# Kernel optimization log

Measured on AMD Instinct MI355X. Metric: run time of the kernel, lower is better.

## Reference

```python
import jax, jax.numpy as jnp
import numpy as np

HEADS = 4

def _axial_attn(xs, wqkv, wproj, bproj, heads=HEADS):
    # xs: [B', C, L]; wqkv: [3C, C]; wproj: [C, C]; bproj: [C]
    Bp, C, L = xs.shape
    hd = C // heads
    scale = hd ** -0.5
    qkv = jnp.einsum('oc,bcl->bol', wqkv, xs)  # [B', 3C, L]
    q, k, v = jnp.split(qkv, 3, axis=1)
    q = q.reshape(Bp, heads, hd, L)
    k = k.reshape(Bp, heads, hd, L)
    v = v.reshape(Bp, heads, hd, L)
    attn = jax.nn.softmax(jnp.einsum('bhdi,bhdj->bhij', q, k) * scale, axis=-1)
    out = jnp.einsum('bhij,bhdj->bhdi', attn, v).reshape(Bp, C, L)
    return jnp.einsum('oc,bcl->bol', wproj, out) + bproj[None, :, None]

def setup_inputs() -> dict:
    key = jax.random.key(0)
    ks = jax.random.split(key, 7)
    B, C, H, W = 8, 128, 128, 128
    return {
        'x': jax.random.normal(ks[0], (B, C, H, W), dtype=jnp.float32),
        'wqkv_h': jax.random.normal(ks[1], (3 * C, C), dtype=jnp.float32) * 0.05,
        'wproj_h': jax.random.normal(ks[2], (C, C), dtype=jnp.float32) * 0.05,
        'bproj_h': jax.random.normal(ks[3], (C,), dtype=jnp.float32) * 0.05,
        'wqkv_w': jax.random.normal(ks[4], (3 * C, C), dtype=jnp.float32) * 0.05,
        'wproj_w': jax.random.normal(ks[5], (C, C), dtype=jnp.float32) * 0.05,
        'bproj_w': jax.random.normal(ks[6], (C,), dtype=jnp.float32) * 0.05,
    }

def reference(x, wqkv_h, wproj_h, bproj_h, wqkv_w, wproj_w, bproj_w):
    B, C, H, W = x.shape
    # height pass: rows become batch, attend along W
    xh = x.transpose(0, 2, 1, 3).reshape(B * H, C, W)
    xh = _axial_attn(xh, wqkv_h, wproj_h, bproj_h)
    xh = xh.reshape(B, H, C, W).transpose(0, 2, 1, 3)
    # width pass: cols become batch, attend along H
    xw = x.transpose(0, 3, 1, 2).reshape(B * W, C, H)
    xw = _axial_attn(xw, wqkv_w, wproj_w, bproj_w)
    xw = xw.reshape(B, W, C, H).transpose(0, 2, 3, 1)
    return (xh + xw) / 2
```

## Files before the change

### kernel.cpp

```cpp
#include <hip/hip_runtime.h>
#include <hip/hip_bf16.h>
#include <stdint.h>

typedef __attribute__((ext_vector_type(8))) short short8v;
typedef __attribute__((ext_vector_type(4))) float f32x4;
typedef unsigned short u16;
typedef unsigned int u32;

__device__ __align__(16) u16 g_xTw[8u * 128u * 128u * 128u];
__device__ __align__(16) u16 g_W1 [8u * 128u * 128u * 128u];
__device__ __align__(16) u16 g_W2 [8u * 128u * 128u * 128u];
__device__ __align__(16) u16 g_wqkvP[2u * 49152u];
__device__ __align__(16) u16 g_wpP [2u * 16384u];

#define XST_OFF 0
#define QT_OFF  32768
#define KT_OFF  43008
#define VH_OFF  53248
#define OT_OFF  61952
#define SMEM_BYTES 72192

__device__ __forceinline__ u16 f2bf(float f) {
    u32 b = __float_as_uint(f);
    b += 0x7FFFu + ((b >> 16) & 1u);
    return (u16)(b >> 16);
}
__device__ __forceinline__ u32 pk2(float a, float b) {
    __hip_bfloat162 h = __float22bfloat162_rn(make_float2(a, b));
    union { __hip_bfloat162 h; u32 u; } cv; cv.h = h; return cv.u;
}
__device__ __forceinline__ float bf2f(u16 u) {
    return __uint_as_float(((u32)u) << 16);
}

__global__ __launch_bounds__(512)
void prep_weights(const float* __restrict__ wqkv_h, const float* __restrict__ wproj_h,
                  const float* __restrict__ wqkv_w, const float* __restrict__ wproj_w)
{
    const float QSC = 0.17677669529663687f;
    int id = blockIdx.x * 512 + threadIdx.x;
    if (id < 12288) {
        int p = id / 6144, i2 = id % 6144;
        int h = i2 / 1536, i3 = i2 % 1536;
        int t = i3 / 256,  i4 = i3 % 256;
        int kk = i4 / 64,  lane = i4 % 64;
        int cc = lane & 15, qq = lane >> 4;
        int r96 = t * 16 + cc;
        int g = r96 >> 5, rl = r96 & 31;
        const float* src = (p == 0 ? wqkv_h : wqkv_w) + (g * 128 + h * 32 + rl) * 128 + kk * 32 + qq * 8;
        float4 a = *(const float4*)src;
        float4 c = *(const float4*)(src + 4);
        float s = (g == 0) ? QSC : 1.0f;
        *(uint4*)(g_wqkvP + (size_t)id * 8) =
            make_uint4(pk2(a.x * s, a.y * s), pk2(a.z * s, a.w * s),
                       pk2(c.x * s, c.y * s), pk2(c.z * s, c.w * s));
    } else {
        int id2 = id - 12288;
        int p = id2 / 2048, i2 = id2 % 2048;
        int h = i2 / 512,  i3 = i2 % 512;
        int t = i3 / 64,   lane = i3 % 64;
        int cc = lane & 15, qq = lane >> 4;
        int o = t * 16 + cc;
        const float* src = (p == 0 ? wproj_h : wproj_w) + o * 128 + h * 32 + qq * 8;
        float4 a = *(const float4*)src;
        float4 c = *(const float4*)(src + 4);
        *(uint4*)(g_wpP + (size_t)id2 * 8) =
            make_uint4(pk2(a.x, a.y), pk2(a.z, a.w), pk2(c.x, c.y), pk2(c.z, c.w));
    }
}

__global__ __launch_bounds__(256)
void transpose_x(const float* __restrict__ x)
{
    __shared__ char tsm[32768];
    const int b = blockIdx.x >> 6;
    const int hp = blockIdx.x & 63;
    const int tid = threadIdx.x;
    for (int hh = 0; hh < 2; ++hh) {
        const int h = hp * 2 + hh;
        #pragma unroll
        for (int it = 0; it < 16; ++it) {
            int task = it * 256 + tid;
            int w = task & 127, c4 = task >> 7;
            const float* p = x + (size_t)b * 2097152 + (c4 * 4) * 16384 + h * 128 + w;
            u32 u0 = pk2(p[0], p[16384]);
            u32 u1 = pk2(p[2 * 16384], p[3 * 16384]);
            int off = w * 256 + ((((c4 >> 1) << 4) ^ ((w & 7) << 4)) | ((c4 & 1) << 3));
            *(uint2*)(tsm + off) = make_uint2(u0, u1);
        }
        __syncthreads();
        #pragma unroll
        for (int it = 0; it < 8; ++it) {
            int i = it * 256 + tid;
            int w = i >> 4, c8 = i & 15;
            uint4 v = *(const uint4*)(tsm + w * 256 + ((c8 << 4) ^ ((w & 7) << 4)));
            size_t ds = ((size_t)(b * 128 + w) * 128 + h) * 128 + (((c8 << 4) ^ ((h & 7) << 4)) >> 1);
            *(uint4*)(g_xTw + ds) = v;
        }
        __syncthreads();
    }
}

__global__ __launch_bounds__(512, 4)
void attn_kernel(const float* __restrict__ x,
                 const float* __restrict__ bias_h, const float* __restrict__ bias_w)
{
    extern __shared__ char smem[];
    const int t    = threadIdx.x;
    const int lane = t & 63;
    const int wv   = t >> 6;
    const int cc   = lane & 15;
    const int qq   = lane >> 4;
    const int pass = blockIdx.x >> 10;
    const int b    = (blockIdx.x >> 7) & 7;
    const int row  = blockIdx.x & 127;
    const f32x4 zf4 = (f32x4){0.f, 0.f, 0.f, 0.f};

    if (pass == 0) {
        #pragma unroll
        for (int it = 0; it < 4; ++it) {
            int task = t + 512 * it;
            int l = task & 127, c8 = task >> 7;
            const float* p = x + (size_t)b * 2097152 + (c8 * 8) * 16384 + row * 128 + l;
            u32 u0 = pk2(p[0], p[16384]);
            u32 u1 = pk2(p[2 * 16384], p[3 * 16384]);
            u32 u2 = pk2(p[4 * 16384], p[5 * 16384]);
            u32 u3 = pk2(p[6 * 16384], p[7 * 16384]);
            *(uint4*)(smem + XST_OFF + l * 256 + ((c8 * 16) ^ ((l & 7) << 4))) = make_uint4(u0, u1, u2, u3);
        }
    } else {
        const u16* slab = g_xTw + (size_t)(b * 128 + row) * 16384;
        #pragma unroll
        for (int it = 0; it < 4; ++it) {
            int idx = t + 512 * it;
            *(uint4*)(smem + XST_OFF + idx * 16) = *(const uint4*)(slab + idx * 8);
        }
    }

    const float* bias = pass ? bias_w : bias_h;
    float biasr[4];
    #pragma unroll
    for (int r = 0; r < 4; ++r) biasr[r] = bias[wv * 16 + 4 * qq + r];

    f32x4 yacc[8];
    #pragma unroll
    for (int i = 0; i < 8; ++i) yacc[i] = zf4;

    __syncthreads();

    const int og = wv & 1;
    const int lg = wv >> 1;

    for (int h = 0; h < 4; ++h) {
        const u16* wb  = g_wqkvP + (size_t)(pass * 4 + h) * 12288;
        const u16* wpb = g_wpP   + (size_t)(pass * 4 + h) * 4096 + (wv * 64 + lane) * 8;

        {
            f32x4 acc[3][2];
            #pragma unroll
            for (int ot = 0; ot < 3; ++ot)
                #pragma unroll
                for (int lt = 0; lt < 2; ++lt) acc[ot][lt] = zf4;
            __builtin_amdgcn_s_setprio(1);
            #pragma unroll
            for (int kk = 0; kk < 4; ++kk) {
                short8v A[3], Bf[2];
                #pragma unroll
                for (int ot = 0; ot < 3; ++ot)
                    A[ot] = *(const short8v*)(wb + (((og * 3 + ot) * 4 + kk) * 64 + lane) * 8);
                #pragma unroll
                for (int lt = 0; lt < 2; ++lt) {
                    int l = lg * 32 + lt * 16 + cc;
                    Bf[lt] = *(const short8v*)(smem + XST_OFF + l * 256 + (((kk * 64 + qq * 16)) ^ ((l & 7) << 4)));
                }
                #pragma unroll
                for (int ot = 0; ot < 3; ++ot)
                    #pragma unroll
                    for (int lt = 0; lt < 2; ++lt)
                        acc[ot][lt] = __builtin_amdgcn_mfma_f32_16x16x32_bf16(A[ot], Bf[lt], acc[ot][lt], 0, 0, 0);
            }
            __builtin_amdgcn_s_setprio(0);
            #pragma unroll
            for (int ot = 0; ot < 3; ++ot) {
                int got = og * 3 + ot;
                #pragma unroll
                for (int lt = 0; lt < 2; ++lt) {
                    int l0 = (lg * 2 + lt) * 16 + cc;
                    f32x4 v = acc[ot][lt];
                    if (got < 2) {
                        *(uint2*)(smem + QT_OFF + l0 * 80 + (got * 16 + 4 * qq) * 2) =
                            make_uint2(pk2(v[0], v[1]), pk2(v[2], v[3]));
                    } else if (got < 4) {
                        *(uint2*)(smem + KT_OFF + l0 * 80 + ((got - 2) * 16 + 4 * qq) * 2) =
                            make_uint2(pk2(v[0], v[1]), pk2(v[2], v[3]));
                    } else {
                        int d0 = (got - 4) * 16 + 4 * qq;
                        #pragma unroll
                        for (int r = 0; r < 4; ++r)
                            *(u16*)(smem + VH_OFF + (d0 + r) * 272 + l0 * 2) = f2bf(v[r]);
                    }
                }
            }
        }
        __syncthreads();

        f32x4 sacc[8];
        {
            short8v aq = *(const short8v*)(smem + QT_OFF + (wv * 16 + cc) * 80 + qq * 16);
            __builtin_amdgcn_s_setprio(1);
            #pragma unroll
            for (int jt = 0; jt < 8; ++jt) {
                short8v bk = *(const short8v*)(smem + KT_OFF + (jt * 16 + cc) * 80 + qq * 16);
                sacc[jt] = __builtin_amdgcn_mfma_f32_16x16x32_bf16(bk, aq, zf4, 0, 0, 0);
            }
            __builtin_amdgcn_s_setprio(0);
        }
        float mx = -3.4e38f;
        #pragma unroll
        for (int jt = 0; jt < 8; ++jt)
            #pragma unroll
            for (int r = 0; r < 4; ++r) mx = fmaxf(mx, sacc[jt][r]);
        mx = fmaxf(mx, __shfl_xor(mx, 16));
        mx = fmaxf(mx, __shfl_xor(mx, 32));
        float sm = 0.f;
        #pragma unroll
        for (int jt = 0; jt < 8; ++jt)
            #pragma unroll
            for (int r = 0; r < 4; ++r) {
                float p = exp2f((sacc[jt][r] - mx) * 1.4426950408889634f);
                sacc[jt][r] = p;
                sm += p;
            }
        sm += __shfl_xor(sm, 16);
        sm += __shfl_xor(sm, 32);
        float rden = 1.0f / sm;
        u32 u[8][2];
        #pragma unroll
        for (int jt = 0; jt < 8; ++jt) {
            u[jt][0] = pk2(sacc[jt][0], sacc[jt][1]);
            u[jt][1] = pk2(sacc[jt][2], sacc[jt][3]);
        }

        f32x4 oacc[2] = {zf4, zf4};
        const int base = cc + ((qq & 1) << 5);
        const bool hiT = (qq >> 1) != 0;
        __builtin_amdgcn_s_setprio(1);
        #pragma unroll
        for (int kt = 0; kt < 4; ++kt) {
            int a0 = __shfl((int)u[2 * kt][0], base),      a1 = __shfl((int)u[2 * kt][1], base);
            int a2 = __shfl((int)u[2 * kt][0], base + 16), a3 = __shfl((int)u[2 * kt][1], base + 16);
            int b0 = __shfl((int)u[2 * kt + 1][0], base),      b1 = __shfl((int)u[2 * kt + 1][1], base);
            int b2 = __shfl((int)u[2 * kt + 1][0], base + 16), b3 = __shfl((int)u[2 * kt + 1][1], base + 16);
            union { uint4 u4; short8v s8; } pf;
            pf.u4 = make_uint4((u32)(hiT ? b0 : a0), (u32)(hiT ? b1 : a1),
                               (u32)(hiT ? b2 : a2), (u32)(hiT ? b3 : a3));
            #pragma unroll
            for (int dt = 0; dt < 2; ++dt) {
                short8v vf = *(const short8v*)(smem + VH_OFF + (dt * 16 + cc) * 272 + kt * 64 + qq * 16);
                oacc[dt] = __builtin_amdgcn_mfma_f32_16x16x32_bf16(vf, pf.s8, oacc[dt], 0, 0, 0);
            }
        }
        __builtin_amdgcn_s_setprio(0);
        #pragma unroll
        for (int dt = 0; dt < 2; ++dt) {
            *(uint2*)(smem + OT_OFF + (wv * 16 + cc) * 80 + (dt * 16 + 4 * qq) * 2) =
                make_uint2(pk2(oacc[dt][0] * rden, oacc[dt][1] * rden),
                           pk2(oacc[dt][2] * rden, oacc[dt][3] * rden));
        }
        __syncthreads();

        {
            short8v aw = *(const short8v*)wpb;
            __builtin_amdgcn_s_setprio(1);
            #pragma unroll
            for (int it = 0; it < 8; ++it) {
                short8v of = *(const short8v*)(smem + OT_OFF + (it * 16 + cc) * 80 + qq * 16);
                yacc[it] = __builtin_amdgcn_mfma_f32_16x16x32_bf16(aw, of, yacc[it], 0, 0, 0);
            }
            __builtin_amdgcn_s_setprio(0);
        }
    }

    u16* dst = pass ? g_W2 : g_W1;
    #pragma unroll
    for (int it = 0; it < 8; ++it) {
        #pragma unroll
        for (int r = 0; r < 4; ++r) {
            float y = (yacc[it][r] + biasr[r]) * 0.5f;
            int o = wv * 16 + 4 * qq + r;
            int l = it * 16 + cc;
            size_t idx = ((size_t)(b * 128 + o) * 128 + row) * 128 + l;
            dst[idx] = f2bf(y);
        }
    }
}

__global__ __launch_bounds__(256)
void merge_w(float* __restrict__ out)
{
    __shared__ char msm[128 * 264];
    const int b = blockIdx.x >> 7;
    const int o = blockIdx.x & 127;
    const int tid = threadIdx.x;
    const u16* slab = g_W2 + (size_t)(b * 128 + o) * 16384;
    #pragma unroll
    for (int it = 0; it < 8; ++it) {
        int i = it * 256 + tid;
        int w = i >> 4, h8 = i & 15;
        *(uint4*)(msm + w * 264 + h8 * 16) = *(const uint4*)(slab + w * 128 + h8 * 8);
    }
    __syncthreads();
    const u16* w1p = g_W1 + (size_t)(b * 128 + o) * 16384;
    float* op = out + (size_t)(b * 128 + o) * 16384;
    #pragma unroll
    for (int it = 0; it < 8; ++it) {
        int i = it * 256 + tid;
        int h = i >> 4, w8 = i & 15;
        uint4 w1 = *(const uint4*)(w1p + h * 128 + w8 * 8);
        float f[8];
        #pragma unroll
        for (int k = 0; k < 8; ++k)
            f[k] = bf2f(*(const u16*)(msm + (w8 * 8 + k) * 264 + h * 2));
        float* dp = op + h * 128 + w8 * 8;
        float4 v0, v1;
        v0.x = f[0] + bf2f((u16)(w1.x & 0xFFFF));
        v0.y = f[1] + bf2f((u16)(w1.x >> 16));
        v0.z = f[2] + bf2f((u16)(w1.y & 0xFFFF));
        v0.w = f[3] + bf2f((u16)(w1.y >> 16));
        v1.x = f[4] + bf2f((u16)(w1.z & 0xFFFF));
        v1.y = f[5] + bf2f((u16)(w1.z >> 16));
        v1.z = f[6] + bf2f((u16)(w1.w & 0xFFFF));
        v1.w = f[7] + bf2f((u16)(w1.w >> 16));
        *(float4*)dp = v0;
        *(float4*)(dp + 4) = v1;
    }
}

extern "C" void kernel_launch(void* const* d_in, const int* in_sizes, int n_in,
                              void* d_out, int out_size, void* d_ws, size_t ws_size,
                              hipStream_t stream)
{
    const float* x       = (const float*)d_in[0];
    const float* wqkv_h  = (const float*)d_in[1];
    const float* wproj_h = (const float*)d_in[2];
    const float* bproj_h = (const float*)d_in[3];
    const float* wqkv_w  = (const float*)d_in[4];
    const float* wproj_w = (const float*)d_in[5];
    const float* bproj_w = (const float*)d_in[6];
    float* out = (float*)d_out;

    (void)hipFuncSetAttribute((const void*)attn_kernel,
                              hipFuncAttributeMaxDynamicSharedMemorySize, SMEM_BYTES);

    prep_weights<<<dim3(32), dim3(512), 0, stream>>>(wqkv_h, wproj_h, wqkv_w, wproj_w);
    transpose_x<<<dim3(512), dim3(256), 0, stream>>>(x);
    attn_kernel<<<dim3(2048), dim3(512), SMEM_BYTES, stream>>>(x, bproj_h, bproj_w);
    merge_w<<<dim3(1024), dim3(256), 0, stream>>>(out);
}
```

Measured before the change: 173.6 us.

## Keep Q and attention output in registers, precompute bf16 row slabs for pass 0

```diff
diff --git a/kernel.cpp b/kernel.cpp
--- a/kernel.cpp
+++ b/kernel.cpp
@@ -7,6 +7,7 @@
 typedef unsigned short u16;
 typedef unsigned int u32;
 
+__device__ __align__(16) u16 g_xh [8u * 128u * 128u * 128u];
 __device__ __align__(16) u16 g_xTw[8u * 128u * 128u * 128u];
 __device__ __align__(16) u16 g_W1 [8u * 128u * 128u * 128u];
 __device__ __align__(16) u16 g_W2 [8u * 128u * 128u * 128u];
@@ -14,11 +15,9 @@
 __device__ __align__(16) u16 g_wpP [2u * 16384u];
 
 #define XST_OFF 0
-#define QT_OFF  32768
-#define KT_OFF  43008
-#define VH_OFF  53248
-#define OT_OFF  61952
-#define SMEM_BYTES 72192
+#define KT_OFF  32768
+#define VH_OFF  43008
+#define SMEM_BYTES 51712
 
 __device__ __forceinline__ u16 f2bf(float f) {
     u32 b = __float_as_uint(f);
@@ -92,6 +91,11 @@
         #pragma unroll
         for (int it = 0; it < 8; ++it) {
             int i = it * 256 + tid;
+            *(uint4*)(g_xh + (size_t)(b * 128 + h) * 16384 + i * 8) = *(const uint4*)(tsm + i * 16);
+        }
+        #pragma unroll
+        for (int it = 0; it < 8; ++it) {
+            int i = it * 256 + tid;
             int w = i >> 4, c8 = i & 15;
             uint4 v = *(const uint4*)(tsm + w * 256 + ((c8 << 4) ^ ((w & 7) << 4)));
             size_t ds = ((size_t)(b * 128 + w) * 128 + h) * 128 + (((c8 << 4) ^ ((h & 7) << 4)) >> 1);
@@ -101,9 +105,8 @@
     }
 }
 
-__global__ __launch_bounds__(512, 4)
-void attn_kernel(const float* __restrict__ x,
-                 const float* __restrict__ bias_h, const float* __restrict__ bias_w)
+__global__ __launch_bounds__(512, 6)
+void attn_kernel(const float* __restrict__ bias_h, const float* __restrict__ bias_w)
 {
     extern __shared__ char smem[];
     const int t    = threadIdx.x;
@@ -116,20 +119,8 @@
     const int row  = blockIdx.x & 127;
     const f32x4 zf4 = (f32x4){0.f, 0.f, 0.f, 0.f};
 
-    if (pass == 0) {
-        #pragma unroll
-        for (int it = 0; it < 4; ++it) {
-            int task = t + 512 * it;
-            int l = task & 127, c8 = task >> 7;
-            const float* p = x + (size_t)b * 2097152 + (c8 * 8) * 16384 + row * 128 + l;
-            u32 u0 = pk2(p[0], p[16384]);
-            u32 u1 = pk2(p[2 * 16384], p[3 * 16384]);
-            u32 u2 = pk2(p[4 * 16384], p[5 * 16384]);
-            u32 u3 = pk2(p[6 * 16384], p[7 * 16384]);
-            *(uint4*)(smem + XST_OFF + l * 256 + ((c8 * 16) ^ ((l & 7) << 4))) = make_uint4(u0, u1, u2, u3);
-        }
-    } else {
-        const u16* slab = g_xTw + (size_t)(b * 128 + row) * 16384;
+    {
+        const u16* slab = (pass ? g_xTw : g_xh) + (size_t)(b * 128 + row) * 16384;
         #pragma unroll
         for (int it = 0; it < 4; ++it) {
             int idx = t + 512 * it;
@@ -137,84 +128,80 @@
         }
     }
 
-    const float* bias = pass ? bias_w : bias_h;
-    float biasr[4];
-    #pragma unroll
-    for (int r = 0; r < 4; ++r) biasr[r] = bias[wv * 16 + 4 * qq + r];
-
     f32x4 yacc[8];
     #pragma unroll
     for (int i = 0; i < 8; ++i) yacc[i] = zf4;
 
     __syncthreads();
 
-    const int og = wv & 1;
-    const int lg = wv >> 1;
+    const int dtk  = wv & 1;
+    const int p0   = wv & 6;
+    const int swz  = (cc & 7) << 4;
+    const int src0 = ((qq & 1) << 5) + cc;
+    const bool hid = (qq >> 1) != 0;
 
     for (int h = 0; h < 4; ++h) {
-        const u16* wb  = g_wqkvP + (size_t)(pass * 4 + h) * 12288;
-        const u16* wpb = g_wpP   + (size_t)(pass * 4 + h) * 4096 + (wv * 64 + lane) * 8;
-
+        const u16* wb = g_wqkvP + (size_t)(pass * 4 + h) * 12288;
+
+        f32x4 qacc[2] = {zf4, zf4};
+        __builtin_amdgcn_s_setprio(1);
+        #pragma unroll
+        for (int kk = 0; kk < 4; ++kk) {
+            short8v aq0 = *(const short8v*)(wb + ((0 * 4 + kk) * 64 + lane) * 8);
+            short8v aq1 = *(const short8v*)(wb + ((1 * 4 + kk) * 64 + lane) * 8);
+            int rq = wv * 16 + cc;
+            short8v xq = *(const short8v*)(smem + XST_OFF + rq * 256 + ((kk * 64 + qq * 16) ^ swz));
+            qacc[0] = __builtin_amdgcn_mfma_f32_16x16x32_bf16(aq0, xq, qacc[0], 0, 0, 0);
+            qacc[1] = __builtin_amdgcn_mfma_f32_16x16x32_bf16(aq1, xq, qacc[1], 0, 0, 0);
+        }
+        __builtin_amdgcn_s_setprio(0);
+        union { uint4 u4; short8v s8; } qf;
         {
-            f32x4 acc[3][2];
-            #pragma unroll
-            for (int ot = 0; ot < 3; ++ot)
+            u32 q00 = pk2(qacc[0][0], qacc[0][1]), q01 = pk2(qacc[0][2], qacc[0][3]);
+            u32 q10 = pk2(qacc[1][0], qacc[1][1]), q11 = pk2(qacc[1][2], qacc[1][3]);
+            u32 a0 = (u32)__shfl((int)q00, src0),      a1 = (u32)__shfl((int)q01, src0);
+            u32 c0 = (u32)__shfl((int)q10, src0),      c1 = (u32)__shfl((int)q11, src0);
+            u32 b0 = (u32)__shfl((int)q00, src0 + 16), b1 = (u32)__shfl((int)q01, src0 + 16);
+            u32 d0 = (u32)__shfl((int)q10, src0 + 16), d1 = (u32)__shfl((int)q11, src0 + 16);
+            qf.u4 = make_uint4(hid ? c0 : a0, hid ? c1 : a1, hid ? d0 : b0, hid ? d1 : b1);
+        }
+
+        {
+            f32x4 kacc[2] = {zf4, zf4}, vacc[2] = {zf4, zf4};
+            __builtin_amdgcn_s_setprio(1);
+            #pragma unroll
+            for (int kk = 0; kk < 4; ++kk) {
+                short8v ak = *(const short8v*)(wb + (((2 + dtk) * 4 + kk) * 64 + lane) * 8);
+                short8v av = *(const short8v*)(wb + (((4 + dtk) * 4 + kk) * 64 + lane) * 8);
+                int r0 = p0 * 16 + cc;
+                short8v xb0 = *(const short8v*)(smem + XST_OFF + r0 * 256 + ((kk * 64 + qq * 16) ^ swz));
+                short8v xb1 = *(const short8v*)(smem + XST_OFF + (r0 + 16) * 256 + ((kk * 64 + qq * 16) ^ swz));
+                kacc[0] = __builtin_amdgcn_mfma_f32_16x16x32_bf16(ak, xb0, kacc[0], 0, 0, 0);
+                kacc[1] = __builtin_amdgcn_mfma_f32_16x16x32_bf16(ak, xb1, kacc[1], 0, 0, 0);
+                vacc[0] = __builtin_amdgcn_mfma_f32_16x16x32_bf16(av, xb0, vacc[0], 0, 0, 0);
+                vacc[1] = __builtin_amdgcn_mfma_f32_16x16x32_bf16(av, xb1, vacc[1], 0, 0, 0);
+            }
+            __builtin_amdgcn_s_setprio(0);
+            #pragma unroll
+            for (int p = 0; p < 2; ++p) {
+                int j = (p0 + p) * 16 + cc;
+                *(uint2*)(smem + KT_OFF + j * 80 + dtk * 32 + 8 * qq) =
+                    make_uint2(pk2(kacc[p][0], kacc[p][1]), pk2(kacc[p][2], kacc[p][3]));
                 #pragma unroll
-                for (int lt = 0; lt < 2; ++lt) acc[ot][lt] = zf4;
-            __builtin_amdgcn_s_setprio(1);
-            #pragma unroll
-            for (int kk = 0; kk < 4; ++kk) {
-                short8v A[3], Bf[2];
-                #pragma unroll
-                for (int ot = 0; ot < 3; ++ot)
-                    A[ot] = *(const short8v*)(wb + (((og * 3 + ot) * 4 + kk) * 64 + lane) * 8);
-                #pragma unroll
-                for (int lt = 0; lt < 2; ++lt) {
-                    int l = lg * 32 + lt * 16 + cc;
-                    Bf[lt] = *(const short8v*)(smem + XST_OFF + l * 256 + (((kk * 64 + qq * 16)) ^ ((l & 7) << 4)));
-                }
-                #pragma unroll
-                for (int ot = 0; ot < 3; ++ot)
-                    #pragma unroll
-                    for (int lt = 0; lt < 2; ++lt)
-                        acc[ot][lt] = __builtin_amdgcn_mfma_f32_16x16x32_bf16(A[ot], Bf[lt], acc[ot][lt], 0, 0, 0);
-            }
-            __builtin_amdgcn_s_setprio(0);
-            #pragma unroll
-            for (int ot = 0; ot < 3; ++ot) {
-                int got = og * 3 + ot;
-                #pragma unroll
-                for (int lt = 0; lt < 2; ++lt) {
-                    int l0 = (lg * 2 + lt) * 16 + cc;
-                    f32x4 v = acc[ot][lt];
-                    if (got < 2) {
-                        *(uint2*)(smem + QT_OFF + l0 * 80 + (got * 16 + 4 * qq) * 2) =
-                            make_uint2(pk2(v[0], v[1]), pk2(v[2], v[3]));
-                    } else if (got < 4) {
-                        *(uint2*)(smem + KT_OFF + l0 * 80 + ((got - 2) * 16 + 4 * qq) * 2) =
-                            make_uint2(pk2(v[0], v[1]), pk2(v[2], v[3]));
-                    } else {
-                        int d0 = (got - 4) * 16 + 4 * qq;
-                        #pragma unroll
-                        for (int r = 0; r < 4; ++r)
-                            *(u16*)(smem + VH_OFF + (d0 + r) * 272 + l0 * 2) = f2bf(v[r]);
-                    }
-                }
+                for (int r = 0; r < 4; ++r)
+                    *(u16*)(smem + VH_OFF + (dtk * 16 + 4 * qq + r) * 272 + j * 2) = f2bf(vacc[p][r]);
             }
         }
         __syncthreads();
 
         f32x4 sacc[8];
-        {
-            short8v aq = *(const short8v*)(smem + QT_OFF + (wv * 16 + cc) * 80 + qq * 16);
-            __builtin_amdgcn_s_setprio(1);
-            #pragma unroll
-            for (int jt = 0; jt < 8; ++jt) {
-                short8v bk = *(const short8v*)(smem + KT_OFF + (jt * 16 + cc) * 80 + qq * 16);
-                sacc[jt] = __builtin_amdgcn_mfma_f32_16x16x32_bf16(bk, aq, zf4, 0, 0, 0);
-            }
-            __builtin_amdgcn_s_setprio(0);
-        }
+        __builtin_amdgcn_s_setprio(1);
+        #pragma unroll
+        for (int jt = 0; jt < 8; ++jt) {
+            short8v kf = *(const short8v*)(smem + KT_OFF + (jt * 16 + cc) * 80 + qq * 16);
+            sacc[jt] = __builtin_amdgcn_mfma_f32_16x16x32_bf16(kf, qf.s8, zf4, 0, 0, 0);
+        }
+        __builtin_amdgcn_s_setprio(0);
         float mx = -3.4e38f;
         #pragma unroll
         for (int jt = 0; jt < 8; ++jt)
@@ -242,18 +229,16 @@
         }
 
         f32x4 oacc[2] = {zf4, zf4};
-        const int base = cc + ((qq & 1) << 5);
-        const bool hiT = (qq >> 1) != 0;
         __builtin_amdgcn_s_setprio(1);
         #pragma unroll
         for (int kt = 0; kt < 4; ++kt) {
-            int a0 = __shfl((int)u[2 * kt][0], base),      a1 = __shfl((int)u[2 * kt][1], base);
-            int a2 = __shfl((int)u[2 * kt][0], base + 16), a3 = __shfl((int)u[2 * kt][1], base + 16);
-            int b0 = __shfl((int)u[2 * kt + 1][0], base),      b1 = __shfl((int)u[2 * kt + 1][1], base);
-            int b2 = __shfl((int)u[2 * kt + 1][0], base + 16), b3 = __shfl((int)u[2 * kt + 1][1], base + 16);
+            int a0 = __shfl((int)u[2 * kt][0], src0),      a1 = __shfl((int)u[2 * kt][1], src0);
+            int a2 = __shfl((int)u[2 * kt][0], src0 + 16), a3 = __shfl((int)u[2 * kt][1], src0 + 16);
+            int b0 = __shfl((int)u[2 * kt + 1][0], src0),      b1 = __shfl((int)u[2 * kt + 1][1], src0);
+            int b2 = __shfl((int)u[2 * kt + 1][0], src0 + 16), b3 = __shfl((int)u[2 * kt + 1][1], src0 + 16);
             union { uint4 u4; short8v s8; } pf;
-            pf.u4 = make_uint4((u32)(hiT ? b0 : a0), (u32)(hiT ? b1 : a1),
-                               (u32)(hiT ? b2 : a2), (u32)(hiT ? b3 : a3));
+            pf.u4 = make_uint4((u32)(hid ? b0 : a0), (u32)(hid ? b1 : a1),
+                               (u32)(hid ? b2 : a2), (u32)(hid ? b3 : a3));
             #pragma unroll
             for (int dt = 0; dt < 2; ++dt) {
                 short8v vf = *(const short8v*)(smem + VH_OFF + (dt * 16 + cc) * 272 + kt * 64 + qq * 16);
@@ -261,34 +246,43 @@
             }
         }
         __builtin_amdgcn_s_setprio(0);
-        #pragma unroll
-        for (int dt = 0; dt < 2; ++dt) {
-            *(uint2*)(smem + OT_OFF + (wv * 16 + cc) * 80 + (dt * 16 + 4 * qq) * 2) =
-                make_uint2(pk2(oacc[dt][0] * rden, oacc[dt][1] * rden),
-                           pk2(oacc[dt][2] * rden, oacc[dt][3] * rden));
-        }
-        __syncthreads();
-
+
+        union { uint4 u4; short8v s8; } of;
         {
-            short8v aw = *(const short8v*)wpb;
+            u32 o00 = pk2(oacc[0][0] * rden, oacc[0][1] * rden);
+            u32 o01 = pk2(oacc[0][2] * rden, oacc[0][3] * rden);
+            u32 o10 = pk2(oacc[1][0] * rden, oacc[1][1] * rden);
+            u32 o11 = pk2(oacc[1][2] * rden, oacc[1][3] * rden);
+            u32 a0 = (u32)__shfl((int)o00, src0),      a1 = (u32)__shfl((int)o01, src0);
+            u32 c0 = (u32)__shfl((int)o10, src0),      c1 = (u32)__shfl((int)o11, src0);
+            u32 b0 = (u32)__shfl((int)o00, src0 + 16), b1 = (u32)__shfl((int)o01, src0 + 16);
+            u32 d0 = (u32)__shfl((int)o10, src0 + 16), d1 = (u32)__shfl((int)o11, src0 + 16);
+            of.u4 = make_uint4(hid ? c0 : a0, hid ? c1 : a1, hid ? d0 : b0, hid ? d1 : b1);
+        }
+        {
+            const u16* wpb = g_wpP + (size_t)(pass * 4 + h) * 4096;
             __builtin_amdgcn_s_setprio(1);
             #pragma unroll
-            for (int it = 0; it < 8; ++it) {
-                short8v of = *(const short8v*)(smem + OT_OFF + (it * 16 + cc) * 80 + qq * 16);
-                yacc[it] = __builtin_amdgcn_mfma_f32_16x16x32_bf16(aw, of, yacc[it], 0, 0, 0);
+            for (int ot = 0; ot < 8; ++ot) {
+                short8v aw = *(const short8v*)(wpb + ((size_t)(ot * 64 + lane)) * 8);
+                yacc[ot] = __builtin_amdgcn_mfma_f32_16x16x32_bf16(aw, of.s8, yacc[ot], 0, 0, 0);
             }
             __builtin_amdgcn_s_setprio(0);
         }
-    }
-
+        if (h < 3) __syncthreads();
+    }
+
+    const float* bias = pass ? bias_w : bias_h;
     u16* dst = pass ? g_W2 : g_W1;
+    const int l = wv * 16 + cc;
     #pragma unroll
-    for (int it = 0; it < 8; ++it) {
+    for (int ot = 0; ot < 8; ++ot) {
+        float4 bb = *(const float4*)(bias + ot * 16 + 4 * qq);
+        float bbr[4] = {bb.x, bb.y, bb.z, bb.w};
         #pragma unroll
         for (int r = 0; r < 4; ++r) {
-            float y = (yacc[it][r] + biasr[r]) * 0.5f;
-            int o = wv * 16 + 4 * qq + r;
-            int l = it * 16 + cc;
+            float y = (yacc[ot][r] + bbr[r]) * 0.5f;
+            int o = ot * 16 + 4 * qq + r;
             size_t idx = ((size_t)(b * 128 + o) * 128 + row) * 128 + l;
             dst[idx] = f2bf(y);
         }
@@ -354,6 +348,6 @@
 
     prep_weights<<<dim3(32), dim3(512), 0, stream>>>(wqkv_h, wproj_h, wqkv_w, wproj_w);
     transpose_x<<<dim3(512), dim3(256), 0, stream>>>(x);
-    attn_kernel<<<dim3(2048), dim3(512), SMEM_BYTES, stream>>>(x, bproj_h, bproj_w);
+    attn_kernel<<<dim3(2048), dim3(512), SMEM_BYTES, stream>>>(bproj_h, bproj_w);
     merge_w<<<dim3(1024), dim3(256), 0, stream>>>(out);
 }
```

Result: slower. 244.6 us (+40.9%).
